# Performance work log

Measured on AMD Instinct MI355X. Metric: run time of the kernel, lower is better.

## Reference

```python
import jax, jax.numpy as jnp
import numpy as np

B = 65536
STATE_DIM = 96
ACTION_DIM = 32
IN_FEATURES = STATE_DIM + ACTION_DIM  # 128
HIDDEN = 256
NUM_HEADS = 200
OUT_FEATURES = 1


def setup_inputs() -> dict:
    key = jax.random.key(0)
    ks = jax.random.split(key, 9)
    state = jax.random.normal(ks[0], (B, STATE_DIM), dtype=jnp.float32)
    action = jax.random.normal(ks[1], (B, ACTION_DIM), dtype=jnp.float32)
    alphas = jax.random.uniform(ks[2], (NUM_HEADS,), dtype=jnp.float32)
    W1 = jax.random.normal(ks[3], (HIDDEN, IN_FEATURES), dtype=jnp.float32) * 0.05
    b1 = jax.random.normal(ks[4], (HIDDEN,), dtype=jnp.float32) * 0.05
    W2 = jax.random.normal(ks[5], (HIDDEN, HIDDEN), dtype=jnp.float32) * 0.05
    b2 = jax.random.normal(ks[6], (HIDDEN,), dtype=jnp.float32) * 0.05
    # stacked head params: heads[h] is Linear(256 -> out_features)
    Wh = jax.random.normal(ks[7], (NUM_HEADS, OUT_FEATURES, HIDDEN), dtype=jnp.float32) * 0.05
    bh = jax.random.normal(ks[8], (NUM_HEADS, OUT_FEATURES), dtype=jnp.float32) * 0.05
    return {"state": state, "action": action, "alphas": alphas,
            "W1": W1, "b1": b1, "W2": W2, "b2": b2, "Wh": Wh, "bh": bh}


def reference(state, action, alphas, W1, b1, W2, b2, Wh, bh):
    x = jnp.concatenate([state, action], axis=1)          # [B, 128]
    x = jax.nn.relu(x @ W1.T + b1)                         # [B, 256]
    x = jax.nn.relu(x @ W2.T + b2)                         # [B, 256]
    # sum_h alpha_h * (x @ Wh[h].T + bh[h])  ==  x @ (sum_h alpha_h Wh[h]).T + sum_h alpha_h bh[h]
    Wc = jnp.einsum('h,hod->od', alphas, Wh)               # [out, 256]
    bc = jnp.einsum('h,ho->o', alphas, bh)                 # [out]
    return x @ Wc.T + bc                                   # [B, out]
```

## Files before the change

kernel.cpp:

```cpp
#include <hip/hip_runtime.h>
#include <hip/hip_bf16.h>


#define B_TOTAL 65536
#define SDIM 96
#define ADIM 32
#define IN_F 128
#define HID 256
#define NHEADS 200
#define BM 64
#define XS_PITCH 136
#define H1_PITCH 264

typedef __bf16 bf16;
typedef __attribute__((ext_vector_type(8))) __bf16 bf16x8;
typedef __attribute__((ext_vector_type(4))) float f32x4;

__global__ void prep_kernel(const float* __restrict__ W1, const float* __restrict__ W2,
                            const float* __restrict__ alphas, const float* __restrict__ Wh,
                            const float* __restrict__ bh,
                            bf16* __restrict__ W1bf, bf16* __restrict__ W2bf,
                            float* __restrict__ Wc) {
    int tid = blockIdx.x * blockDim.x + threadIdx.x;
    if (tid < IN_F * HID) W1bf[tid] = (bf16)W1[tid];
    if (tid < HID * HID)  W2bf[tid] = (bf16)W2[tid];
    if (tid < HID) {
        float acc = 0.f;
        for (int h = 0; h < NHEADS; ++h) acc += alphas[h] * Wh[h * HID + tid];
        Wc[tid] = acc;
    }
    if (tid == HID) {
        float acc = 0.f;
        for (int h = 0; h < NHEADS; ++h) acc += alphas[h] * bh[h];
        Wc[HID] = acc;
    }
}

__global__ __launch_bounds__(256, 2) void critic_kernel(
        const float* __restrict__ state, const float* __restrict__ action,
        const float* __restrict__ b1, const float* __restrict__ b2,
        const bf16* __restrict__ W1bf, const bf16* __restrict__ W2bf,
        const float* __restrict__ Wc, float* __restrict__ out) {

    __shared__ bf16 xs[BM * XS_PITCH];
    __shared__ bf16 h1s[BM * H1_PITCH];
    __shared__ float sWc[HID];
    __shared__ float sPart[4][BM];

    const int tid  = threadIdx.x;
    const int wave = tid >> 6;
    const int lane = tid & 63;
    const int q    = lane >> 4;
    const int ln   = lane & 15;
    const int colw = wave * 64;
    const int row0 = blockIdx.x * BM;

    sWc[tid] = Wc[tid];

    #pragma unroll
    for (int i = 0; i < 8; ++i) {
        int idx = tid + i * 256;
        int r   = idx >> 5;
        int c4  = idx & 31;
        float4 v;
        if (c4 < 24) v = ((const float4*)(state  + (size_t)(row0 + r) * SDIM))[c4];
        else         v = ((const float4*)(action + (size_t)(row0 + r) * ADIM))[c4 - 24];
        bf16* dst = &xs[r * XS_PITCH + c4 * 4];
        dst[0] = (bf16)v.x; dst[1] = (bf16)v.y; dst[2] = (bf16)v.z; dst[3] = (bf16)v.w;
    }
    __syncthreads();

    f32x4 acc[4][4];
    #pragma unroll
    for (int mt = 0; mt < 4; ++mt)
        #pragma unroll
        for (int nt = 0; nt < 4; ++nt)
            acc[mt][nt] = (f32x4){0.f, 0.f, 0.f, 0.f};

    #pragma unroll
    for (int ks = 0; ks < 4; ++ks) {
        const int k0 = ks * 32 + q * 8;
        bf16x8 a[4], b[4];
        #pragma unroll
        for (int mt = 0; mt < 4; ++mt)
            a[mt] = *(const bf16x8*)&xs[(mt * 16 + ln) * XS_PITCH + k0];
        #pragma unroll
        for (int nt = 0; nt < 4; ++nt)
            b[nt] = *(const bf16x8*)&W1bf[(size_t)(colw + nt * 16 + ln) * IN_F + k0];
        #pragma unroll
        for (int mt = 0; mt < 4; ++mt)
            #pragma unroll
            for (int nt = 0; nt < 4; ++nt)
                acc[mt][nt] = __builtin_amdgcn_mfma_f32_16x16x32_bf16(a[mt], b[nt], acc[mt][nt], 0, 0, 0);
    }

    #pragma unroll
    for (int nt = 0; nt < 4; ++nt) {
        const int n    = colw + nt * 16 + ln;
        const float bias = b1[n];
        #pragma unroll
        for (int mt = 0; mt < 4; ++mt)
            #pragma unroll
            for (int r = 0; r < 4; ++r) {
                float v = acc[mt][nt][r] + bias;
                v = v > 0.f ? v : 0.f;
                h1s[(mt * 16 + q * 4 + r) * H1_PITCH + n] = (bf16)v;
            }
    }
    __syncthreads();

    #pragma unroll
    for (int mt = 0; mt < 4; ++mt)
        #pragma unroll
        for (int nt = 0; nt < 4; ++nt)
            acc[mt][nt] = (f32x4){0.f, 0.f, 0.f, 0.f};

    #pragma unroll
    for (int ks = 0; ks < 8; ++ks) {
        const int k0 = ks * 32 + q * 8;
        bf16x8 a[4], b[4];
        #pragma unroll
        for (int mt = 0; mt < 4; ++mt)
            a[mt] = *(const bf16x8*)&h1s[(mt * 16 + ln) * H1_PITCH + k0];
        #pragma unroll
        for (int nt = 0; nt < 4; ++nt)
            b[nt] = *(const bf16x8*)&W2bf[(size_t)(colw + nt * 16 + ln) * HID + k0];
        #pragma unroll
        for (int mt = 0; mt < 4; ++mt)
            #pragma unroll
            for (int nt = 0; nt < 4; ++nt)
                acc[mt][nt] = __builtin_amdgcn_mfma_f32_16x16x32_bf16(a[mt], b[nt], acc[mt][nt], 0, 0, 0);
    }

    float partial[4][4];
    #pragma unroll
    for (int mt = 0; mt < 4; ++mt)
        #pragma unroll
        for (int r = 0; r < 4; ++r)
            partial[mt][r] = 0.f;

    #pragma unroll
    for (int nt = 0; nt < 4; ++nt) {
        const int n     = colw + nt * 16 + ln;
        const float bias = b2[n];
        const float wc   = sWc[n];
        #pragma unroll
        for (int mt = 0; mt < 4; ++mt)
            #pragma unroll
            for (int r = 0; r < 4; ++r) {
                float v = acc[mt][nt][r] + bias;
                v = v > 0.f ? v : 0.f;
                partial[mt][r] += v * wc;
            }
    }

    #pragma unroll
    for (int off = 1; off < 16; off <<= 1)
        #pragma unroll
        for (int mt = 0; mt < 4; ++mt)
            #pragma unroll
            for (int r = 0; r < 4; ++r)
                partial[mt][r] += __shfl_xor(partial[mt][r], off, 64);

    if (ln == 0) {
        #pragma unroll
        for (int mt = 0; mt < 4; ++mt)
            #pragma unroll
            for (int r = 0; r < 4; ++r)
                sPart[wave][mt * 16 + q * 4 + r] = partial[mt][r];
    }
    __syncthreads();

    if (tid < BM) {
        float v = sPart[0][tid] + sPart[1][tid] + sPart[2][tid] + sPart[3][tid] + Wc[HID];
        out[row0 + tid] = v;
    }
}

extern "C" void kernel_launch(void* const* d_in, const int* in_sizes, int n_in,
                              void* d_out, int out_size, void* d_ws, size_t ws_size,
                              hipStream_t stream) {
    const float* state  = (const float*)d_in[0];
    const float* action = (const float*)d_in[1];
    const float* alphas = (const float*)d_in[2];
    const float* W1     = (const float*)d_in[3];
    const float* b1     = (const float*)d_in[4];
    const float* W2     = (const float*)d_in[5];
    const float* b2     = (const float*)d_in[6];
    const float* Wh     = (const float*)d_in[7];
    const float* bh     = (const float*)d_in[8];
    float* out = (float*)d_out;

    bf16*  W1bf = (bf16*)d_ws;
    bf16*  W2bf = (bf16*)((char*)d_ws + 65536);
    float* Wc   = (float*)((char*)d_ws + 65536 + 131072);

    prep_kernel<<<256, 256, 0, stream>>>(W1, W2, alphas, Wh, bh, W1bf, W2bf, Wc);
    critic_kernel<<<B_TOTAL / BM, 256, 0, stream>>>(state, action, b1, b2, W1bf, W2bf, Wc, out);
}
```

Before: 128.1 us.

## Keep weights in registers and loop over multiple row tiles per block

Each block now processes four 64-row tiles, loading W1/W2 fragments, biases and combined head weights into registers once and reusing them across tiles. The next tile's inputs are prefetched into registers while the current tile computes, and input staging uses 8-wide bf16 stores. This removes repeated global weight fetches per tile but raises register pressure substantially and lowers occupancy to one block per CU with a quarter of the blocks.

After: 117.4 us. -8.3%, faster.

```diff
diff --git a/kernel.cpp b/kernel.cpp
--- a/kernel.cpp
+++ b/kernel.cpp
@@ -9,8 +9,9 @@
 #define HID 256
 #define NHEADS 200
 #define BM 64
+#define NTILES 4
 #define XS_PITCH 136
-#define H1_PITCH 264
+#define H1_PITCH 260
 
 typedef __bf16 bf16;
 typedef __attribute__((ext_vector_type(8))) __bf16 bf16x8;
@@ -26,6 +27,7 @@
     if (tid < HID * HID)  W2bf[tid] = (bf16)W2[tid];
     if (tid < HID) {
         float acc = 0.f;
+        #pragma unroll 8
         for (int h = 0; h < NHEADS; ++h) acc += alphas[h] * Wh[h * HID + tid];
         Wc[tid] = acc;
     }
@@ -36,7 +38,7 @@
     }
 }
 
-__global__ __launch_bounds__(256, 2) void critic_kernel(
+__global__ __launch_bounds__(256, 1) void critic_kernel(
         const float* __restrict__ state, const float* __restrict__ action,
         const float* __restrict__ b1, const float* __restrict__ b2,
         const bf16* __restrict__ W1bf, const bf16* __restrict__ W2bf,
@@ -44,7 +46,6 @@
 
     __shared__ bf16 xs[BM * XS_PITCH];
     __shared__ bf16 h1s[BM * H1_PITCH];
-    __shared__ float sWc[HID];
     __shared__ float sPart[4][BM];
 
     const int tid  = threadIdx.x;
@@ -53,127 +54,170 @@
     const int q    = lane >> 4;
     const int ln   = lane & 15;
     const int colw = wave * 64;
-    const int row0 = blockIdx.x * BM;
-
-    sWc[tid] = Wc[tid];
-
+    const int brow0 = blockIdx.x * (BM * NTILES);
+
+    bf16x8 w1f[4][4];
     #pragma unroll
-    for (int i = 0; i < 8; ++i) {
-        int idx = tid + i * 256;
-        int r   = idx >> 5;
-        int c4  = idx & 31;
-        float4 v;
-        if (c4 < 24) v = ((const float4*)(state  + (size_t)(row0 + r) * SDIM))[c4];
-        else         v = ((const float4*)(action + (size_t)(row0 + r) * ADIM))[c4 - 24];
-        bf16* dst = &xs[r * XS_PITCH + c4 * 4];
-        dst[0] = (bf16)v.x; dst[1] = (bf16)v.y; dst[2] = (bf16)v.z; dst[3] = (bf16)v.w;
-    }
-    __syncthreads();
-
-    f32x4 acc[4][4];
+    for (int ks = 0; ks < 4; ++ks)
+        #pragma unroll
+        for (int nt = 0; nt < 4; ++nt)
+            w1f[ks][nt] = *(const bf16x8*)&W1bf[(size_t)(colw + nt * 16 + ln) * IN_F + ks * 32 + q * 8];
+
+    bf16x8 w2f[8][4];
     #pragma unroll
-    for (int mt = 0; mt < 4; ++mt)
+    for (int ks = 0; ks < 8; ++ks)
         #pragma unroll
         for (int nt = 0; nt < 4; ++nt)
-            acc[mt][nt] = (f32x4){0.f, 0.f, 0.f, 0.f};
-
-    #pragma unroll
-    for (int ks = 0; ks < 4; ++ks) {
-        const int k0 = ks * 32 + q * 8;
-        bf16x8 a[4], b[4];
-        #pragma unroll
-        for (int mt = 0; mt < 4; ++mt)
-            a[mt] = *(const bf16x8*)&xs[(mt * 16 + ln) * XS_PITCH + k0];
-        #pragma unroll
-        for (int nt = 0; nt < 4; ++nt)
-            b[nt] = *(const bf16x8*)&W1bf[(size_t)(colw + nt * 16 + ln) * IN_F + k0];
-        #pragma unroll
-        for (int mt = 0; mt < 4; ++mt)
-            #pragma unroll
-            for (int nt = 0; nt < 4; ++nt)
-                acc[mt][nt] = __builtin_amdgcn_mfma_f32_16x16x32_bf16(a[mt], b[nt], acc[mt][nt], 0, 0, 0);
-    }
-
+            w2f[ks][nt] = *(const bf16x8*)&W2bf[(size_t)(colw + nt * 16 + ln) * HID + ks * 32 + q * 8];
+
+    float b1v[4], b2v[4], wcv[4];
     #pragma unroll
     for (int nt = 0; nt < 4; ++nt) {
-        const int n    = colw + nt * 16 + ln;
-        const float bias = b1[n];
+        const int n = colw + nt * 16 + ln;
+        b1v[nt] = b1[n];
+        b2v[nt] = b2[n];
+        wcv[nt] = Wc[n];
+    }
+    const float bc = Wc[HID];
+
+    float4 px[4][2];
+    {
+        const int row0 = brow0;
+        #pragma unroll
+        for (int i = 0; i < 4; ++i) {
+            const int idx = tid + i * 256;
+            const int r   = idx >> 4;
+            const int c8  = idx & 15;
+            const float* src = (c8 < 12) ? (state  + (size_t)(row0 + r) * SDIM + c8 * 8)
+                                         : (action + (size_t)(row0 + r) * ADIM + (c8 - 12) * 8);
+            px[i][0] = ((const float4*)src)[0];
+            px[i][1] = ((const float4*)src)[1];
+        }
+    }
+
+    for (int t = 0; t < NTILES; ++t) {
+        const int row0 = brow0 + t * BM;
+
+        #pragma unroll
+        for (int i = 0; i < 4; ++i) {
+            const int idx = tid + i * 256;
+            const int r   = idx >> 4;
+            const int c8  = idx & 15;
+            bf16x8 v = (bf16x8){(bf16)px[i][0].x, (bf16)px[i][0].y, (bf16)px[i][0].z, (bf16)px[i][0].w,
+                                (bf16)px[i][1].x, (bf16)px[i][1].y, (bf16)px[i][1].z, (bf16)px[i][1].w};
+            *(bf16x8*)&xs[r * XS_PITCH + c8 * 8] = v;
+        }
+        __syncthreads();
+
+        if (t + 1 < NTILES) {
+            const int nrow0 = row0 + BM;
+            #pragma unroll
+            for (int i = 0; i < 4; ++i) {
+                const int idx = tid + i * 256;
+                const int r   = idx >> 4;
+                const int c8  = idx & 15;
+                const float* src = (c8 < 12) ? (state  + (size_t)(nrow0 + r) * SDIM + c8 * 8)
+                                             : (action + (size_t)(nrow0 + r) * ADIM + (c8 - 12) * 8);
+                px[i][0] = ((const float4*)src)[0];
+                px[i][1] = ((const float4*)src)[1];
+            }
+        }
+
+        f32x4 acc[4][4];
         #pragma unroll
         for (int mt = 0; mt < 4; ++mt)
             #pragma unroll
-            for (int r = 0; r < 4; ++r) {
-                float v = acc[mt][nt][r] + bias;
-                v = v > 0.f ? v : 0.f;
-                h1s[(mt * 16 + q * 4 + r) * H1_PITCH + n] = (bf16)v;
-            }
-    }
-    __syncthreads();
-
-    #pragma unroll
-    for (int mt = 0; mt < 4; ++mt)
-        #pragma unroll
-        for (int nt = 0; nt < 4; ++nt)
-            acc[mt][nt] = (f32x4){0.f, 0.f, 0.f, 0.f};
-
-    #pragma unroll
-    for (int ks = 0; ks < 8; ++ks) {
-        const int k0 = ks * 32 + q * 8;
-        bf16x8 a[4], b[4];
+            for (int nt = 0; nt < 4; ++nt)
+                acc[mt][nt] = (f32x4){0.f, 0.f, 0.f, 0.f};
+
+        #pragma unroll
+        for (int ks = 0; ks < 4; ++ks) {
+            const int k0 = ks * 32 + q * 8;
+            bf16x8 a[4];
+            #pragma unroll
+            for (int mt = 0; mt < 4; ++mt)
+                a[mt] = *(const bf16x8*)&xs[(mt * 16 + ln) * XS_PITCH + k0];
+            #pragma unroll
+            for (int mt = 0; mt < 4; ++mt)
+                #pragma unroll
+                for (int nt = 0; nt < 4; ++nt)
+                    acc[mt][nt] = __builtin_amdgcn_mfma_f32_16x16x32_bf16(a[mt], w1f[ks][nt], acc[mt][nt], 0, 0, 0);
+        }
+
+        #pragma unroll
+        for (int nt = 0; nt < 4; ++nt) {
+            const int n = colw + nt * 16 + ln;
+            #pragma unroll
+            for (int mt = 0; mt < 4; ++mt)
+                #pragma unroll
+                for (int r = 0; r < 4; ++r) {
+                    float v = acc[mt][nt][r] + b1v[nt];
+                    v = v > 0.f ? v : 0.f;
+                    h1s[(mt * 16 + q * 4 + r) * H1_PITCH + n] = (bf16)v;
+                }
+        }
+        __syncthreads();
+
         #pragma unroll
         for (int mt = 0; mt < 4; ++mt)
-            a[mt] = *(const bf16x8*)&h1s[(mt * 16 + ln) * H1_PITCH + k0];
-        #pragma unroll
-        for (int nt = 0; nt < 4; ++nt)
-            b[nt] = *(const bf16x8*)&W2bf[(size_t)(colw + nt * 16 + ln) * HID + k0];
+            #pragma unroll
+            for (int nt = 0; nt < 4; ++nt)
+                acc[mt][nt] = (f32x4){0.f, 0.f, 0.f, 0.f};
+
+        #pragma unroll
+        for (int ks = 0; ks < 8; ++ks) {
+            const int k0 = ks * 32 + q * 8;
+            bf16x8 a[4];
+            #pragma unroll
+            for (int mt = 0; mt < 4; ++mt)
+                a[mt] = *(const bf16x8*)&h1s[(mt * 16 + ln) * H1_PITCH + k0];
+            #pragma unroll
+            for (int mt = 0; mt < 4; ++mt)
+                #pragma unroll
+                for (int nt = 0; nt < 4; ++nt)
+                    acc[mt][nt] = __builtin_amdgcn_mfma_f32_16x16x32_bf16(a[mt], w2f[ks][nt], acc[mt][nt], 0, 0, 0);
+        }
+
+        float partial[4][4];
         #pragma unroll
         for (int mt = 0; mt < 4; ++mt)
             #pragma unroll
-            for (int nt = 0; nt < 4; ++nt)
-                acc[mt][nt] = __builtin_amdgcn_mfma_f32_16x16x32_bf16(a[mt], b[nt], acc[mt][nt], 0, 0, 0);
-    }
-
-    float partial[4][4];
-    #pragma unroll
-    for (int mt = 0; mt < 4; ++mt)
-        #pragma unroll
-        for (int r = 0; r < 4; ++r)
-            partial[mt][r] = 0.f;
-
-    #pragma unroll
-    for (int nt = 0; nt < 4; ++nt) {
-        const int n     = colw + nt * 16 + ln;
-        const float bias = b2[n];
-        const float wc   = sWc[n];
-        #pragma unroll
-        for (int mt = 0; mt < 4; ++mt)
-            #pragma unroll
-            for (int r = 0; r < 4; ++r) {
-                float v = acc[mt][nt][r] + bias;
-                v = v > 0.f ? v : 0.f;
-                partial[mt][r] += v * wc;
-            }
-    }
-
-    #pragma unroll
-    for (int off = 1; off < 16; off <<= 1)
-        #pragma unroll
-        for (int mt = 0; mt < 4; ++mt)
-            #pragma unroll
             for (int r = 0; r < 4; ++r)
-                partial[mt][r] += __shfl_xor(partial[mt][r], off, 64);
-
-    if (ln == 0) {
-        #pragma unroll
-        for (int mt = 0; mt < 4; ++mt)
-            #pragma unroll
-            for (int r = 0; r < 4; ++r)
-                sPart[wave][mt * 16 + q * 4 + r] = partial[mt][r];
-    }
-    __syncthreads();
-
-    if (tid < BM) {
-        float v = sPart[0][tid] + sPart[1][tid] + sPart[2][tid] + sPart[3][tid] + Wc[HID];
-        out[row0 + tid] = v;
+                partial[mt][r] = 0.f;
+
+        #pragma unroll
+        for (int nt = 0; nt < 4; ++nt) {
+            #pragma unroll
+            for (int mt = 0; mt < 4; ++mt)
+                #pragma unroll
+                for (int r = 0; r < 4; ++r) {
+                    float v = acc[mt][nt][r] + b2v[nt];
+                    v = v > 0.f ? v : 0.f;
+                    partial[mt][r] += v * wcv[nt];
+                }
+        }
+
+        #pragma unroll
+        for (int off = 1; off < 16; off <<= 1)
+            #pragma unroll
+            for (int mt = 0; mt < 4; ++mt)
+                #pragma unroll
+                for (int r = 0; r < 4; ++r)
+                    partial[mt][r] += __shfl_xor(partial[mt][r], off, 64);
+
+        if (ln == 0) {
+            #pragma unroll
+            for (int mt = 0; mt < 4; ++mt)
+                #pragma unroll
+                for (int r = 0; r < 4; ++r)
+                    sPart[wave][mt * 16 + q * 4 + r] = partial[mt][r];
+        }
+        __syncthreads();
+
+        if (tid < BM) {
+            float v = sPart[0][tid] + sPart[1][tid] + sPart[2][tid] + sPart[3][tid] + bc;
+            out[row0 + tid] = v;
+        }
     }
 }
 
@@ -196,5 +240,5 @@
     float* Wc   = (float*)((char*)d_ws + 65536 + 131072);
 
     prep_kernel<<<256, 256, 0, stream>>>(W1, W2, alphas, Wh, bh, W1bf, W2bf, Wc);
-    critic_kernel<<<B_TOTAL / BM, 256, 0, stream>>>(state, action, b1, b2, W1bf, W2bf, Wc, out);
+    critic_kernel<<<B_TOTAL / (BM * NTILES), 256, 0, stream>>>(state, action, b1, b2, W1bf, W2bf, Wc, out);
 }
```
